# Kernel optimization log

Measured on AMD Instinct MI355X. Metric: run time of the kernel, lower is better.

## Reference

```python
import jax, jax.numpy as jnp
import numpy as np

BANDS, ROWS, SIM_THRESH = 16, 8, 0.5


def setup_inputs() -> dict:
    key = jax.random.key(0)
    k1, k2 = jax.random.split(key)
    N, D = 8192, 256
    Z = jax.random.normal(k1, (N, D), dtype=jnp.float32)
    # random hyperplanes ~ N(0, I), (bands*rows, D) -- sampled once (torch samples in forward)
    planes = jax.random.normal(k2, (BANDS * ROWS, D), dtype=jnp.float32)
    return {"Z": Z, "planes": planes}


def reference(Z, planes):
    N, D = Z.shape
    # signature: sign of projections, (bands, rows, N); +/-1 vs bool is equivalent for bucketing
    sig_bits = (planes @ Z.T >= 0).reshape(BANDS, ROWS, N)
    # bit-pack each band's row-signature into an integer key == hashing the signature bytes
    bit_weights = (2 ** jnp.arange(ROWS)).astype(jnp.int32)
    keys = jnp.einsum('brn,r->bn', sig_bits.astype(jnp.int32), bit_weights)  # (bands, N)
    # cosine pairwise similarity (row-normalized GEMM)
    Zn = Z / jnp.linalg.norm(Z, axis=1, keepdims=True)
    sim = Zn @ Zn.T  # (N, N)
    # number of bands in which i and j fall in the same LSH bucket
    def band_match(acc, k):
        return acc + (k[:, None] == k[None, :]).astype(jnp.float32), None
    counts, _ = jax.lax.scan(band_match, jnp.zeros((N, N), jnp.float32), keys)
    # original masks the diagonal with -inf, thresholds at sim_thresh, and emits one
    # (sim) entry per matching band into an uncoalesced sparse tensor; densified this
    # is counts * sim on surviving off-diagonal pairs.
    mask = (sim >= SIM_THRESH) & (~jnp.eye(N, dtype=bool))
    return jnp.where(mask, counts * sim, 0.0)
```

## Files before the change

kernel.cpp:

```cpp
#include <hip/hip_runtime.h>

typedef __attribute__((ext_vector_type(4))) float floatx4;

#define N_PTS 8192
#define D_DIM 256
#define N_PLANES 128
#define BANDS 16
#define ROWS 8
#define NTILE 64
#define FILL_BLOCKS 2048

__device__ inline void load_lds16(const void* g, void* l) {
    __builtin_amdgcn_global_load_lds(
        (const __attribute__((address_space(1))) unsigned int*)g,
        (__attribute__((address_space(3))) unsigned int*)l, 16, 0, 0);
}

__device__ inline float dot4(float4 a, float4 b) {
    return a.x * b.x + a.y * b.y + a.z * b.z + a.w * b.w;
}

__global__ __launch_bounds__(256) void fill_norm_kernel(
    const float* __restrict__ Z, unsigned char* __restrict__ Zn,
    float* __restrict__ out) {
    int t = threadIdx.x;

    if (blockIdx.x < N_PTS / 16) {
        int base = blockIdx.x * 16;
        int row = t >> 4, ch = t & 15;
        const float4* zp =
            (const float4*)(Z + (size_t)(base + row) * D_DIM + ch * 16);
        float4 z0 = zp[0], z1 = zp[1], z2 = zp[2], z3 = zp[3];

        float ss = dot4(z0, z0) + dot4(z1, z1) + dot4(z2, z2) + dot4(z3, z3);
#pragma unroll
        for (int off = 8; off > 0; off >>= 1) ss += __shfl_xor(ss, off);
        float inv = rsqrtf(ss);
        int4 o;
        int p;
        p = __builtin_amdgcn_cvt_pk_fp8_f32(z0.x * inv, z0.y * inv, 0, false);
        o.x = __builtin_amdgcn_cvt_pk_fp8_f32(z0.z * inv, z0.w * inv, p, true);
        p = __builtin_amdgcn_cvt_pk_fp8_f32(z1.x * inv, z1.y * inv, 0, false);
        o.y = __builtin_amdgcn_cvt_pk_fp8_f32(z1.z * inv, z1.w * inv, p, true);
        p = __builtin_amdgcn_cvt_pk_fp8_f32(z2.x * inv, z2.y * inv, 0, false);
        o.z = __builtin_amdgcn_cvt_pk_fp8_f32(z2.z * inv, z2.w * inv, p, true);
        p = __builtin_amdgcn_cvt_pk_fp8_f32(z3.x * inv, z3.y * inv, 0, false);
        o.w = __builtin_amdgcn_cvt_pk_fp8_f32(z3.z * inv, z3.w * inv, p, true);
        *(int4*)(Zn + (size_t)(base + row) * D_DIM + ch * 16) = o;
    }

    floatx4 z4 = {0.f, 0.f, 0.f, 0.f};
    floatx4* outv = (floatx4*)out + (size_t)blockIdx.x * 8192 + t;
#pragma unroll
    for (int i = 0; i < 32; ++i)
        __builtin_nontemporal_store(z4, outv + (size_t)i * 256);
}

__global__ __launch_bounds__(256, 4) void gemm_kernel(
    const unsigned char* __restrict__ Zn, const float* __restrict__ Z,
    const float* __restrict__ planes, float* __restrict__ out) {
    __shared__ __align__(16) unsigned char As[16384];
    __shared__ __align__(16) unsigned char Bs[16384];

    int idx = blockIdx.x;
    int bi = (int)((129.0f - sqrtf(16641.0f - 8.0f * (float)idx)) * 0.5f);
    while ((bi + 1) * NTILE - ((bi + 1) * bi) / 2 <= idx) ++bi;
    while (bi * NTILE - (bi * (bi - 1)) / 2 > idx) --bi;
    int bj = bi + (idx - (bi * NTILE - (bi * (bi - 1)) / 2));
    int rowBase = bi * 128;
    int colBase = bj * 128;
    bool diag = (bi == bj);

    int t = threadIdx.x;
    const unsigned char* ZnA = Zn + (size_t)rowBase * D_DIM;
    const unsigned char* ZnB = Zn + (size_t)colBase * D_DIM;

    int wave = t >> 6, lane = t & 63;
    int wm = wave >> 1, wn = wave & 1;
    int quad = lane >> 4, l16 = lane & 15;

    floatx4 acc[4][4] = {};

    for (int s = 0; s < 2; ++s) {
        __syncthreads();
#pragma unroll
        for (int i = 0; i < 4; ++i) {
            int sa = i * 256 + t;
            int c = sa >> 7, row = sa & 127;
            size_t gOff = (size_t)row * D_DIM + s * 128 + c * 16;
            load_lds16(ZnA + gOff, &As[sa * 16]);
            load_lds16(ZnB + gOff, &Bs[sa * 16]);
        }
        __syncthreads();

#pragma unroll
        for (int k2 = 0; k2 < 4; ++k2) {
            int kByte = k2 * 32 + quad * 8;
            int cc = kByte >> 4;
            int off8 = kByte & 8;
            long afr[4], bfr[4];
#pragma unroll
            for (int mt = 0; mt < 4; ++mt)
                afr[mt] = *(const long*)&As[(cc * 128 + wm * 64 + mt * 16 + l16) * 16 + off8];
#pragma unroll
            for (int nt = 0; nt < 4; ++nt)
                bfr[nt] = *(const long*)&Bs[(cc * 128 + wn * 64 + nt * 16 + l16) * 16 + off8];
#pragma unroll
            for (int mt = 0; mt < 4; ++mt)
#pragma unroll
                for (int nt = 0; nt < 4; ++nt)
                    acc[mt][nt] = __builtin_amdgcn_mfma_f32_16x16x32_fp8_fp8(
                        afr[mt], bfr[nt], acc[mt][nt], 0, 0, 0);
        }
    }

    bool any = false;
#pragma unroll
    for (int mt = 0; mt < 4; ++mt)
#pragma unroll
        for (int nt = 0; nt < 4; ++nt)
#pragma unroll
            for (int r = 0; r < 4; ++r) {
                int gi = rowBase + wm * 64 + mt * 16 + quad * 4 + r;
                int gj = colBase + wn * 64 + nt * 16 + l16;
                any = any || (acc[mt][nt][r] >= 0.5f && gi != gj);
            }

    if (__ballot(any)) {
#pragma unroll
        for (int mt = 0; mt < 4; ++mt)
#pragma unroll
            for (int nt = 0; nt < 4; ++nt) {
                int gj = colBase + wn * 64 + nt * 16 + l16;
#pragma unroll
                for (int r = 0; r < 4; ++r) {
                    int gi = rowBase + wm * 64 + mt * 16 + quad * 4 + r;
                    float s = acc[mt][nt][r];
                    if (s >= 0.5f && gi != gj) {
                        const float* zi = Z + (size_t)gi * D_DIM;
                        const float* zj = Z + (size_t)gj * D_DIM;
                        int c = 0;
#pragma clang loop unroll(disable)
                        for (int b = 0; b < BANDS; ++b) {
                            bool same = true;
#pragma clang loop unroll(disable)
                            for (int rr = 0; rr < ROWS; ++rr) {
                                const float* pl =
                                    planes + (size_t)(b * ROWS + rr) * D_DIM;
                                float di = 0.f, dj = 0.f;
#pragma clang loop unroll(disable)
                                for (int k = 0; k < D_DIM; ++k) {
                                    float pv = pl[k];
                                    di += pv * zi[k];
                                    dj += pv * zj[k];
                                }
                                same = same && ((di >= 0.f) == (dj >= 0.f));
                            }
                            c += same ? 1 : 0;
                        }
                        float v = s * (float)c;
                        out[(size_t)gi * N_PTS + gj] = v;
                        if (!diag) out[(size_t)gj * N_PTS + gi] = v;
                    }
                }
            }
    }
}

extern "C" void kernel_launch(void* const* d_in, const int* in_sizes, int n_in,
                              void* d_out, int out_size, void* d_ws,
                              size_t ws_size, hipStream_t stream) {
    const float* Z = (const float*)d_in[0];
    const float* planes = (const float*)d_in[1];
    float* out = (float*)d_out;

    unsigned char* Zn = (unsigned char*)d_ws;

    fill_norm_kernel<<<FILL_BLOCKS, 256, 0, stream>>>(Z, Zn, out);
    int nblocks = NTILE * (NTILE + 1) / 2;
    gemm_kernel<<<nblocks, 256, 0, stream>>>(Zn, Z, planes, out);
}
```

Baseline: 293.7 us.

## Defer LSH band matching to a compacted survivor list and fuse output zeroing into GEMM

Moves the per-pair band-signature recomputation out of the GEMM epilogue. The GEMM now appends surviving (i, j, sim) triples to a workspace list through an atomic counter, and a separate small scatter kernel computes band matches and writes both symmetric entries. The output zero-fill moves from the norm kernel into the first 2048 GEMM blocks, using plain stores, so it can overlap with MFMA work. This removes divergent long scalar loops that stall GEMM waves, at the cost of an extra launch, atomics, and a survivor cap of 131072. The scatter kernel runs on only 16 blocks and there is no ordering between the zero stores and the scattered writes, so correctness depends on the GEMM kernel finishing before the scatter runs.

```diff
diff --git a/kernel.cpp b/kernel.cpp
--- a/kernel.cpp
+++ b/kernel.cpp
@@ -4,11 +4,11 @@
 
 #define N_PTS 8192
 #define D_DIM 256
-#define N_PLANES 128
 #define BANDS 16
 #define ROWS 8
 #define NTILE 64
-#define FILL_BLOCKS 2048
+#define MAX_SURV 131072
+#define FILL_SLICES 2048
 
 __device__ inline void load_lds16(const void* g, void* l) {
     __builtin_amdgcn_global_load_lds(
@@ -20,45 +20,37 @@
     return a.x * b.x + a.y * b.y + a.z * b.z + a.w * b.w;
 }
 
-__global__ __launch_bounds__(256) void fill_norm_kernel(
-    const float* __restrict__ Z, unsigned char* __restrict__ Zn,
-    float* __restrict__ out) {
+__global__ __launch_bounds__(256) void norm_kernel(const float* __restrict__ Z,
+                                                   unsigned char* __restrict__ Zn,
+                                                   int* __restrict__ cnt) {
     int t = threadIdx.x;
-
-    if (blockIdx.x < N_PTS / 16) {
-        int base = blockIdx.x * 16;
-        int row = t >> 4, ch = t & 15;
-        const float4* zp =
-            (const float4*)(Z + (size_t)(base + row) * D_DIM + ch * 16);
-        float4 z0 = zp[0], z1 = zp[1], z2 = zp[2], z3 = zp[3];
-
-        float ss = dot4(z0, z0) + dot4(z1, z1) + dot4(z2, z2) + dot4(z3, z3);
-#pragma unroll
-        for (int off = 8; off > 0; off >>= 1) ss += __shfl_xor(ss, off);
-        float inv = rsqrtf(ss);
-        int4 o;
-        int p;
-        p = __builtin_amdgcn_cvt_pk_fp8_f32(z0.x * inv, z0.y * inv, 0, false);
-        o.x = __builtin_amdgcn_cvt_pk_fp8_f32(z0.z * inv, z0.w * inv, p, true);
-        p = __builtin_amdgcn_cvt_pk_fp8_f32(z1.x * inv, z1.y * inv, 0, false);
-        o.y = __builtin_amdgcn_cvt_pk_fp8_f32(z1.z * inv, z1.w * inv, p, true);
-        p = __builtin_amdgcn_cvt_pk_fp8_f32(z2.x * inv, z2.y * inv, 0, false);
-        o.z = __builtin_amdgcn_cvt_pk_fp8_f32(z2.z * inv, z2.w * inv, p, true);
-        p = __builtin_amdgcn_cvt_pk_fp8_f32(z3.x * inv, z3.y * inv, 0, false);
-        o.w = __builtin_amdgcn_cvt_pk_fp8_f32(z3.z * inv, z3.w * inv, p, true);
-        *(int4*)(Zn + (size_t)(base + row) * D_DIM + ch * 16) = o;
-    }
-
-    floatx4 z4 = {0.f, 0.f, 0.f, 0.f};
-    floatx4* outv = (floatx4*)out + (size_t)blockIdx.x * 8192 + t;
-#pragma unroll
-    for (int i = 0; i < 32; ++i)
-        __builtin_nontemporal_store(z4, outv + (size_t)i * 256);
+    if (blockIdx.x == 0 && t == 0) *cnt = 0;
+    int base = blockIdx.x * 16;
+    int row = t >> 4, ch = t & 15;
+
+    const float4* zp = (const float4*)(Z + (size_t)(base + row) * D_DIM + ch * 16);
+    float4 z0 = zp[0], z1 = zp[1], z2 = zp[2], z3 = zp[3];
+
+    float ss = dot4(z0, z0) + dot4(z1, z1) + dot4(z2, z2) + dot4(z3, z3);
+#pragma unroll
+    for (int off = 8; off > 0; off >>= 1) ss += __shfl_xor(ss, off);
+    float inv = rsqrtf(ss);
+    int4 o;
+    int p;
+    p = __builtin_amdgcn_cvt_pk_fp8_f32(z0.x * inv, z0.y * inv, 0, false);
+    o.x = __builtin_amdgcn_cvt_pk_fp8_f32(z0.z * inv, z0.w * inv, p, true);
+    p = __builtin_amdgcn_cvt_pk_fp8_f32(z1.x * inv, z1.y * inv, 0, false);
+    o.y = __builtin_amdgcn_cvt_pk_fp8_f32(z1.z * inv, z1.w * inv, p, true);
+    p = __builtin_amdgcn_cvt_pk_fp8_f32(z2.x * inv, z2.y * inv, 0, false);
+    o.z = __builtin_amdgcn_cvt_pk_fp8_f32(z2.z * inv, z2.w * inv, p, true);
+    p = __builtin_amdgcn_cvt_pk_fp8_f32(z3.x * inv, z3.y * inv, 0, false);
+    o.w = __builtin_amdgcn_cvt_pk_fp8_f32(z3.z * inv, z3.w * inv, p, true);
+    *(int4*)(Zn + (size_t)(base + row) * D_DIM + ch * 16) = o;
 }
 
 __global__ __launch_bounds__(256, 4) void gemm_kernel(
-    const unsigned char* __restrict__ Zn, const float* __restrict__ Z,
-    const float* __restrict__ planes, float* __restrict__ out) {
+    const unsigned char* __restrict__ Zn, float* __restrict__ out,
+    int* __restrict__ cnt, int4* __restrict__ surv) {
     __shared__ __align__(16) unsigned char As[16384];
     __shared__ __align__(16) unsigned char Bs[16384];
 
@@ -69,7 +61,6 @@
     int bj = bi + (idx - (bi * NTILE - (bi * (bi - 1)) / 2));
     int rowBase = bi * 128;
     int colBase = bj * 128;
-    bool diag = (bi == bj);
 
     int t = threadIdx.x;
     const unsigned char* ZnA = Zn + (size_t)rowBase * D_DIM;
@@ -114,6 +105,13 @@
         }
     }
 
+    if (idx < FILL_SLICES) {
+        floatx4 z4 = {0.f, 0.f, 0.f, 0.f};
+        floatx4* outv = (floatx4*)out + (size_t)idx * 8192 + t;
+#pragma unroll
+        for (int i = 0; i < 32; ++i) outv[(size_t)i * 256] = z4;
+    }
+
     bool any = false;
 #pragma unroll
     for (int mt = 0; mt < 4; ++mt)
@@ -137,33 +135,53 @@
                     int gi = rowBase + wm * 64 + mt * 16 + quad * 4 + r;
                     float s = acc[mt][nt][r];
                     if (s >= 0.5f && gi != gj) {
-                        const float* zi = Z + (size_t)gi * D_DIM;
-                        const float* zj = Z + (size_t)gj * D_DIM;
-                        int c = 0;
-#pragma clang loop unroll(disable)
-                        for (int b = 0; b < BANDS; ++b) {
-                            bool same = true;
-#pragma clang loop unroll(disable)
-                            for (int rr = 0; rr < ROWS; ++rr) {
-                                const float* pl =
-                                    planes + (size_t)(b * ROWS + rr) * D_DIM;
-                                float di = 0.f, dj = 0.f;
-#pragma clang loop unroll(disable)
-                                for (int k = 0; k < D_DIM; ++k) {
-                                    float pv = pl[k];
-                                    di += pv * zi[k];
-                                    dj += pv * zj[k];
-                                }
-                                same = same && ((di >= 0.f) == (dj >= 0.f));
-                            }
-                            c += same ? 1 : 0;
+                        int slot = atomicAdd(cnt, 1);
+                        if (slot < MAX_SURV) {
+                            int4 e;
+                            e.x = gi; e.y = gj;
+                            e.z = __float_as_int(s); e.w = 0;
+                            surv[slot] = e;
                         }
-                        float v = s * (float)c;
-                        out[(size_t)gi * N_PTS + gj] = v;
-                        if (!diag) out[(size_t)gj * N_PTS + gi] = v;
                     }
                 }
             }
+    }
+}
+
+__global__ __launch_bounds__(256) void scatter_kernel(
+    const int* __restrict__ cnt, const int4* __restrict__ surv,
+    const float* __restrict__ Z, const float* __restrict__ planes,
+    float* __restrict__ out) {
+    int n = *cnt;
+    if (n > MAX_SURV) n = MAX_SURV;
+    for (int e = blockIdx.x * blockDim.x + threadIdx.x; e < n;
+         e += gridDim.x * blockDim.x) {
+        int4 sv = surv[e];
+        int gi = sv.x, gj = sv.y;
+        float s = __int_as_float(sv.z);
+        const float* zi = Z + (size_t)gi * D_DIM;
+        const float* zj = Z + (size_t)gj * D_DIM;
+        int c = 0;
+#pragma clang loop unroll(disable)
+        for (int b = 0; b < BANDS; ++b) {
+            bool same = true;
+#pragma clang loop unroll(disable)
+            for (int rr = 0; rr < ROWS; ++rr) {
+                const float* pl = planes + (size_t)(b * ROWS + rr) * D_DIM;
+                float di = 0.f, dj = 0.f;
+#pragma clang loop unroll(disable)
+                for (int k = 0; k < D_DIM; ++k) {
+                    float pv = pl[k];
+                    di += pv * zi[k];
+                    dj += pv * zj[k];
+                }
+                same = same && ((di >= 0.f) == (dj >= 0.f));
+            }
+            c += same ? 1 : 0;
+        }
+        float v = s * (float)c;
+        out[(size_t)gi * N_PTS + gj] = v;
+        out[(size_t)gj * N_PTS + gi] = v;
     }
 }
 
@@ -175,8 +193,11 @@
     float* out = (float*)d_out;
 
     unsigned char* Zn = (unsigned char*)d_ws;
-
-    fill_norm_kernel<<<FILL_BLOCKS, 256, 0, stream>>>(Z, Zn, out);
+    int* cnt = (int*)((char*)d_ws + (size_t)N_PTS * D_DIM);
+    int4* surv = (int4*)((char*)d_ws + (size_t)N_PTS * D_DIM + 16);
+
+    norm_kernel<<<N_PTS / 16, 256, 0, stream>>>(Z, Zn, cnt);
     int nblocks = NTILE * (NTILE + 1) / 2;
-    gemm_kernel<<<nblocks, 256, 0, stream>>>(Zn, Z, planes, out);
-}
+    gemm_kernel<<<nblocks, 256, 0, stream>>>(Zn, out, cnt, surv);
+    scatter_kernel<<<16, 256, 0, stream>>>(cnt, surv, Z, planes, out);
+}
```

After: 283.9 us. 3.3% less time.
